# Optimization experiments

Measured on AMD Instinct MI355X. Metric: run time of the kernel, lower is better.

Reference implementation:

```python
import jax, jax.numpy as jnp
import numpy as np

B, T, C = 4, 2048, 1024
H = 16  # NUM_HEADS
HD = C // H  # head_dim = 64


def setup_inputs() -> dict:
    key = jax.random.key(0)
    k1, k2, k3 = jax.random.split(key, 3)
    x = jax.random.normal(k1, (B, T, C), dtype=jnp.float32)
    # nn.Linear weights: stored as [out, in]; apply as x @ W.T
    W_attn = jax.random.normal(k2, (3 * C, C), dtype=jnp.float32) * (1.0 / np.sqrt(C))
    W_proj = jax.random.normal(k3, (C, C), dtype=jnp.float32) * (1.0 / np.sqrt(C))
    return {"x": x, "W_attn": W_attn, "W_proj": W_proj}


def reference(x, W_attn, W_proj):
    Bv, Tv, Cv = x.shape
    qkv = x @ W_attn.T  # [B, T, 3C]
    q, k, v = jnp.split(qkv, 3, axis=2)
    # [B, H, T, HD]
    q = q.reshape(Bv, Tv, H, HD).transpose(0, 2, 1, 3)
    k = k.reshape(Bv, Tv, H, HD).transpose(0, 2, 1, 3)
    v = v.reshape(Bv, Tv, H, HD).transpose(0, 2, 1, 3)
    att = jnp.einsum("bhqd,bhkd->bhqk", q, k) * (1.0 / np.sqrt(HD))
    causal = jnp.tril(jnp.ones((Tv, Tv), dtype=bool))
    att = jnp.where(causal[None, None, :, :], att, -jnp.inf)
    att = jax.nn.softmax(att, axis=-1)
    y = jnp.einsum("bhqk,bhkd->bhqd", att, v)
    y = y.transpose(0, 2, 1, 3).reshape(Bv, Tv, Cv)
    return y @ W_proj.T
```

## Files before the change

### kernel.cpp

```cpp
#include <hip/hip_runtime.h>

typedef _Float16 f16;
typedef _Float16 half8 __attribute__((ext_vector_type(8)));
typedef _Float16 half4v __attribute__((ext_vector_type(4)));
typedef __fp16 fp16x2 __attribute__((ext_vector_type(2)));
typedef float floatx4 __attribute__((ext_vector_type(4)));
typedef unsigned int uint;

constexpr int Bsz = 4, Tseq = 2048, Cdim = 1024, NH = 16, HDim = 64;
constexpr int Mtok = Bsz * Tseq;
constexpr int NQT = Tseq / 64;
constexpr float QSCALE = 0.18033688f;

#define GLDS16(src, dst) __builtin_amdgcn_global_load_lds( \
    (const __attribute__((address_space(1))) void*)(src),  \
    (__attribute__((address_space(3))) void*)(dst), 16, 0, 0)

__device__ __forceinline__ float fexp2(float x) { return __builtin_amdgcn_exp2f(x); }
__device__ __forceinline__ uint pkrtz(float a, float b) {
  fp16x2 h = __builtin_amdgcn_cvt_pkrtz(a, b);
  return __builtin_bit_cast(uint, h);
}
#define MFMA16(a, b, c) __builtin_amdgcn_mfma_f32_16x16x32_f16((a), (b), (c), 0, 0, 0)

__global__ void cvt3_kernel(const float* __restrict__ x, const float* __restrict__ wa,
                            const float* __restrict__ wp,
                            f16* __restrict__ xh, f16* __restrict__ wah, f16* __restrict__ wph) {
  constexpr int nx = Mtok * Cdim, nwa = 3 * Cdim * Cdim, nwp = Cdim * Cdim;
  int i = (blockIdx.x * blockDim.x + threadIdx.x) * 4;
  const float* src; f16* dst; int off;
  if (i < nx)            { src = x;  dst = xh;  off = i; }
  else if (i < nx + nwa) { src = wa; dst = wah; off = i - nx; }
  else                   { src = wp; dst = wph; off = i - nx - nwa; }
  float4 v = *(const float4*)(src + off);
  half4v o;
  o[0] = (f16)v.x; o[1] = (f16)v.y; o[2] = (f16)v.z; o[3] = (f16)v.w;
  *(half4v*)(dst + off) = o;
}

__global__ __launch_bounds__(512, 2)
void qk8p_kernel(const f16* __restrict__ X, const f16* __restrict__ W,
                 f16* __restrict__ q_out, f16* __restrict__ k_out)
{
  __shared__ __align__(16) char smem[131072];
  constexpr int K = 1024, NT = 16;
  const int sbid = (blockIdx.x & 7) * 32 + (blockIdx.x >> 3);
  const int bm = sbid >> 3, bn = sbid & 7;
  const int m0 = bm * 256, n0 = bn * 256;
  const int tid = threadIdx.x, w = tid >> 6, lane = tid & 63;
  const int wr = w >> 2, wc = w & 3;
  const int g = lane >> 4, lm = lane & 15;

  const int grow = lane >> 3;
  const int cg = (lane & 7) ^ grow;

  auto stage_half = [&](int op, int t, int h) {
    const f16* src = op ? W : X;
    char* base = smem + op * 65536 + (t & 1) * 32768 + h * 16384;
    const int rbase = (op ? n0 : m0) + h * 128;
#pragma unroll
    for (int r2 = 0; r2 < 2; ++r2) {
      int row = rbase + r2 * 64 + w * 8 + grow;
      GLDS16(src + (size_t)row * K + t * 64 + cg * 8,
             base + (r2 * 64 + w * 8) * 128);
    }
  };

  floatx4 acc[8][4];
#pragma unroll
  for (int i = 0; i < 8; ++i)
#pragma unroll
    for (int j = 0; j < 4; ++j) acc[i][j] = (floatx4)0.0f;

  const int sw = lm & 7;
  const char* S = smem;
  const int Abase = wr * 16384 + lm * 128;
  const int Bbase = 65536 + (wc >> 1) * 16384 + ((wc & 1) * 64 + lm) * 128;

  half8 a0[4][2], a1[4][2], b0[2][2], b1[2][2];

  stage_half(0, 0, 0); stage_half(0, 0, 1);
  stage_half(1, 0, 0); stage_half(1, 0, 1);
  stage_half(1, 1, 0); stage_half(1, 1, 1);

#pragma unroll 2
  for (int t = 0; t < NT; ++t) {
    const int par = (t & 1) * 32768;

    if (t == NT - 1) { asm volatile("s_waitcnt vmcnt(0)" ::: "memory"); }
    else             { asm volatile("s_waitcnt vmcnt(4)" ::: "memory"); }
    __builtin_amdgcn_s_barrier();
#pragma unroll
    for (int i = 0; i < 4; ++i)
#pragma unroll
      for (int kk = 0; kk < 2; ++kk)
        a0[i][kk] = *(const half8*)(S + par + Abase + i * 2048 + 16 * ((kk * 4 + g) ^ sw));
#pragma unroll
    for (int j = 0; j < 2; ++j)
#pragma unroll
      for (int kk = 0; kk < 2; ++kk)
        b0[j][kk] = *(const half8*)(S + par + Bbase + j * 2048 + 16 * ((kk * 4 + g) ^ sw));
    if (t + 1 < NT) stage_half(0, t + 1, 0);
    asm volatile("s_waitcnt lgkmcnt(0)" ::: "memory");
    __builtin_amdgcn_sched_barrier(0);
    __builtin_amdgcn_s_setprio(1);
#pragma unroll
    for (int i = 0; i < 4; ++i)
#pragma unroll
      for (int j = 0; j < 2; ++j)
#pragma unroll
        for (int kk = 0; kk < 2; ++kk)
          acc[i][j] = MFMA16(a0[i][kk], b0[j][kk], acc[i][j]);
    __builtin_amdgcn_s_setprio(0);

    __builtin_amdgcn_s_barrier();
#pragma unroll
    for (int j = 0; j < 2; ++j)
#pragma unroll
      for (int kk = 0; kk < 2; ++kk)
        b1[j][kk] = *(const half8*)(S + par + Bbase + (j + 2) * 2048 + 16 * ((kk * 4 + g) ^ sw));
    if (t + 1 < NT) stage_half(0, t + 1, 1);
    asm volatile("s_waitcnt lgkmcnt(0)" ::: "memory");
    __builtin_amdgcn_sched_barrier(0);
    __builtin_amdgcn_s_setprio(1);
#pragma unroll
    for (int i = 0; i < 4; ++i)
#pragma unroll
      for (int j = 0; j < 2; ++j)
#pragma unroll
        for (int kk = 0; kk < 2; ++kk)
          acc[i][j + 2] = MFMA16(a0[i][kk], b1[j][kk], acc[i][j + 2]);
    __builtin_amdgcn_s_setprio(0);

    __builtin_amdgcn_s_barrier();
#pragma unroll
    for (int i = 0; i < 4; ++i)
#pragma unroll
      for (int kk = 0; kk < 2; ++kk)
        a1[i][kk] = *(const half8*)(S + par + Abase + (i + 4) * 2048 + 16 * ((kk * 4 + g) ^ sw));
    if (t + 2 < NT) stage_half(1, t + 2, 0);
    asm volatile("s_waitcnt lgkmcnt(0)" ::: "memory");
    __builtin_amdgcn_sched_barrier(0);
    __builtin_amdgcn_s_setprio(1);
#pragma unroll
    for (int i = 0; i < 4; ++i)
#pragma unroll
      for (int j = 0; j < 2; ++j)
#pragma unroll
        for (int kk = 0; kk < 2; ++kk)
          acc[i + 4][j + 2] = MFMA16(a1[i][kk], b1[j][kk], acc[i + 4][j + 2]);
    __builtin_amdgcn_s_setprio(0);

    __builtin_amdgcn_s_barrier();
    if (t + 2 < NT) stage_half(1, t + 2, 1);
    __builtin_amdgcn_s_setprio(1);
#pragma unroll
    for (int i = 0; i < 4; ++i)
#pragma unroll
      for (int j = 0; j < 2; ++j)
#pragma unroll
        for (int kk = 0; kk < 2; ++kk)
          acc[i + 4][j] = MFMA16(a1[i][kk], b0[j][kk], acc[i + 4][j]);
    __builtin_amdgcn_s_setprio(0);
  }

#pragma unroll
  for (int i = 0; i < 8; ++i) {
#pragma unroll
    for (int j = 0; j < 4; ++j) {
#pragma unroll
      for (int r = 0; r < 4; ++r) {
        int m = m0 + wr * 128 + i * 16 + 4 * g + r;
        int n = n0 + wc * 64 + j * 16 + lm;
        float v = acc[i][j][r];
        int which = n >> 10;
        int inner = n & 1023;
        int h = inner >> 6, hd = inner & 63;
        int b = m >> 11, t = m & 2047;
        if (which == 0) {
          v *= QSCALE;
          q_out[(((size_t)(b * NH + h)) * Tseq + t) * HDim + hd] = (f16)v;
        } else {
          k_out[(((size_t)(b * NH + h)) * Tseq + t) * HDim + hd] = (f16)v;
        }
      }
    }
  }
}

template<int EPI>
__device__ __forceinline__ void gemm_body(f16* As, f16* Bs,
    const f16* __restrict__ X, const f16* __restrict__ W,
    float* __restrict__ outF, f16* __restrict__ v_out,
    int N, int K, int bm, int bn)
{
  constexpr int BK = 32;
  const int tid = threadIdx.x;
  const int wave = tid >> 6;
  const int lane = tid & 63;
  const int g = lane >> 4, lm = lane & 15;
  const int m0 = bm * 128, n0 = bn * 128;
  const int wr = wave >> 1, wc = wave & 1;

  floatx4 acc[4][4];
#pragma unroll
  for (int i = 0; i < 4; ++i)
#pragma unroll
    for (int j = 0; j < 4; ++j) acc[i][j] = (floatx4)0.0f;

  for (int k0 = 0; k0 < K; k0 += BK) {
    __syncthreads();
#pragma unroll
    for (int t = 0; t < 2; ++t) {
      int row = (wave * 2 + t) * 16 + (lane >> 2);
      int cg = (lane & 3) ^ ((row >> 1) & 3);
      GLDS16(X + (size_t)(m0 + row) * K + k0 + cg * 8,
             (char*)As + (wave * 2 + t) * 1024);
      GLDS16(W + (size_t)(n0 + row) * K + k0 + cg * 8,
             (char*)Bs + (wave * 2 + t) * 1024);
    }
    __syncthreads();

    half8 af[4], bf[4];
#pragma unroll
    for (int i = 0; i < 4; ++i) {
      int rowa = wr * 64 + i * 16 + lm;
      int cga = g ^ ((rowa >> 1) & 3);
      af[i] = *(const half8*)((const char*)As + rowa * 64 + cga * 16);
      int rowb = wc * 64 + i * 16 + lm;
      int cgb = g ^ ((rowb >> 1) & 3);
      bf[i] = *(const half8*)((const char*)Bs + rowb * 64 + cgb * 16);
    }
#pragma unroll
    for (int i = 0; i < 4; ++i)
#pragma unroll
      for (int j = 0; j < 4; ++j)
        acc[i][j] = MFMA16(af[i], bf[j], acc[i][j]);
  }

#pragma unroll
  for (int i = 0; i < 4; ++i) {
#pragma unroll
    for (int j = 0; j < 4; ++j) {
#pragma unroll
      for (int r = 0; r < 4; ++r) {
        int m = m0 + wr * 64 + i * 16 + 4 * g + r;
        int n = n0 + wc * 64 + j * 16 + lm;
        float v = acc[i][j][r];
        if constexpr (EPI == 1) {
          outF[(size_t)m * N + n] = v;
        } else {
          int h = m >> 6, hd = m & 63;
          int b = n >> 11, t = n & 2047;
          v_out[(((size_t)(b * NH + h)) * HDim + hd) * Tseq + t] = (f16)v;
        }
      }
    }
  }
}

__global__ __launch_bounds__(256)
void vt_kernel(const f16* __restrict__ xh, const f16* __restrict__ wVh, f16* __restrict__ Vth) {
  __shared__ __align__(16) f16 As[128 * 32];
  __shared__ __align__(16) f16 Bs[128 * 32];
  int bm = blockIdx.x & 7, bn = blockIdx.x >> 3;
  gemm_body<2>(As, Bs, wVh, xh, nullptr, Vth, Mtok, Cdim, bm, bn);
}

__global__ __launch_bounds__(256)
void proj_kernel(const f16* __restrict__ yh, const f16* __restrict__ wPh, float* __restrict__ out) {
  __shared__ __align__(16) f16 As[128 * 32];
  __shared__ __align__(16) f16 Bs[128 * 32];
  const int x = blockIdx.x & 7;
  const int u = blockIdx.x >> 3;
  int c = u >> 4, ww = u & 15;
  int bm = x * 8 + (c >> 1) * 4 + (ww >> 2);
  int bn = (c & 1) * 4 + (ww & 3);
  gemm_body<1>(As, Bs, yh, wPh, out, nullptr, Cdim, Cdim, bm, bn);
}

__device__ __forceinline__ void softmax_tile(floatx4* s,
                                             bool diag, int j0, int qg, char* pwrow, int g, int lm) {
  if (diag) {
#pragma unroll
    for (int nf = 0; nf < 4; ++nf)
#pragma unroll
      for (int r = 0; r < 4; ++r)
        if (j0 + nf * 16 + 4 * g + r > qg) s[nf][r] = -1e30f;
  }
#pragma unroll
  for (int nf = 0; nf < 4; ++nf) {
    float p0 = fexp2(s[nf][0]), p1 = fexp2(s[nf][1]);
    float p2 = fexp2(s[nf][2]), p3 = fexp2(s[nf][3]);
    uint lo = pkrtz(p0, p1), hi = pkrtz(p2, p3);
    int slot = 2 * nf + (g >> 1);
    uint2 u; u.x = lo; u.y = hi;
    *(uint2*)(pwrow + 16 * (slot ^ (lm & 7)) + 8 * (g & 1)) = u;
  }
}

__device__ __forceinline__ void store_o(const floatx4* acc, const floatx4 l5, int q0w,
                                        int g, int lm, f16* __restrict__ Y, int b, int h) {
#pragma unroll
  for (int r = 0; r < 4; ++r) {
    float inv = 1.0f / l5[r];
    int t = q0w + 4 * g + r;
    size_t base = ((size_t)(b * Tseq + t)) * Cdim + h * HDim;
#pragma unroll
    for (int ng = 0; ng < 4; ++ng)
      Y[base + ng * 16 + lm] = (f16)(acc[ng][r] * inv);
  }
}

__global__ __launch_bounds__(256)
void attn_kernel(const f16* __restrict__ Q, const f16* __restrict__ Kg,
                 const f16* __restrict__ Vt, f16* __restrict__ Y)
{
  __shared__ __align__(16) char smem[40960];
  int wg = blockIdx.x;
  int lin = (wg & 7) * 128 + (wg >> 3);
  const int p  = lin & 15;
  const int bh = lin >> 4;
  const int itB = NQT - p;
  const f16* Qb  = Q  + (size_t)bh * Tseq * HDim;
  const f16* Kb  = Kg + (size_t)bh * Tseq * HDim;
  const f16* Vtb = Vt + (size_t)bh * HDim * Tseq;

  const int tid = threadIdx.x, w = tid >> 6, lane = tid & 63;
  const int g = lane >> 4, lm = lane & 15;
  char* pwrow = smem + 32768 + w * 2048 + lm * 128;
  const int b = bh >> 4, h = bh & 15;

  half8 ones;
#pragma unroll
  for (int i = 0; i < 8; ++i) ones[i] = (f16)1.0f;

  int q0 = (NQT - 1 - p) * 64;
  int qg = q0 + w * 16 + lm;
  half8 qf0 = *(const half8*)(Qb + (size_t)(q0 + w * 16 + lm) * HDim + g * 8);
  half8 qf1 = *(const half8*)(Qb + (size_t)(q0 + w * 16 + lm) * HDim + 32 + g * 8);

  floatx4 acc[4], acc5;
  acc5 = (floatx4)0.f;
#pragma unroll
  for (int ng = 0; ng < 4; ++ng) acc[ng] = (floatx4)0.f;

  const int srow = w * 8 + (lane >> 3);
  const int sslot = lane & 7;

  auto stage = [&](int j0s, int buf) {
#pragma unroll
    for (int t = 0; t < 2; ++t) {
      int row = srow + t * 32;
      int cg = sslot ^ (row & 7);
      GLDS16(Kb + (size_t)(j0s + row) * HDim + cg * 8,
             smem + buf * 8192 + (w * 8 + t * 32) * 128);
      GLDS16(Vtb + (size_t)row * Tseq + j0s + cg * 8,
             smem + 16384 + buf * 8192 + (w * 8 + t * 32) * 128);
    }
  };

  stage(0, 0);
  asm volatile("s_waitcnt vmcnt(0)" ::: "memory");
  __builtin_amdgcn_s_barrier();

  for (int it = 0; it < NQT + 1; ++it) {
    const bool lastB = (it == itB - 1);
    const bool last  = (it == NQT);
    const int jt = (it < itB) ? it : it - itB;
    const int j0 = jt * 64;

    if (!last) {
      const int itn = it + 1;
      const int jtn = (itn < itB) ? itn : itn - itB;
      stage(jtn * 64, itn & 1);
    }

    char* kb   = smem + (it & 1) * 8192;
    char* vbuf = smem + 16384 + (it & 1) * 8192;

    floatx4 s[4];
    __builtin_amdgcn_s_setprio(1);
#pragma unroll
    for (int nf = 0; nf < 4; ++nf) {
      half8 kf0 = *(const half8*)(kb + (nf * 16 + lm) * 128 + 16 * ((g)     ^ (lm & 7)));
      half8 kf1 = *(const half8*)(kb + (nf * 16 + lm) * 128 + 16 * ((4 + g) ^ (lm & 7)));
      s[nf] = MFMA16(kf0, qf0, (floatx4)0.f);
      s[nf] = MFMA16(kf1, qf1, s[nf]);
    }
    __builtin_amdgcn_s_setprio(0);

    softmax_tile(s, lastB || last, j0, qg, pwrow, g, lm);
    half8 pa0 = *(const half8*)(pwrow + 16 * ((g)     ^ (lm & 7)));
    half8 pa1 = *(const half8*)(pwrow + 16 * ((4 + g) ^ (lm & 7)));

    __builtin_amdgcn_s_setprio(1);
    acc5 = MFMA16(pa0, ones, acc5);
    acc5 = MFMA16(pa1, ones, acc5);
#pragma unroll
    for (int c = 0; c < 2; ++c)
#pragma unroll
      for (int ng = 0; ng < 4; ++ng) {
        half8 vbf = *(const half8*)(vbuf + (ng * 16 + lm) * 128 + 16 * ((4 * c + g) ^ (lm & 7)));
        acc[ng] = MFMA16(c ? pa1 : pa0, vbf, acc[ng]);
      }
    __builtin_amdgcn_s_setprio(0);

    asm volatile("s_waitcnt vmcnt(0)" ::: "memory");
    __builtin_amdgcn_s_barrier();

    if (lastB) {
      store_o(acc, acc5, q0 + 16 * w, g, lm, Y, b, h);
      q0 = p * 64;
      qg = q0 + w * 16 + lm;
      qf0 = *(const half8*)(Qb + (size_t)(q0 + w * 16 + lm) * HDim + g * 8);
      qf1 = *(const half8*)(Qb + (size_t)(q0 + w * 16 + lm) * HDim + 32 + g * 8);
      acc5 = (floatx4)0.f;
#pragma unroll
      for (int ng = 0; ng < 4; ++ng) acc[ng] = (floatx4)0.f;
    }
  }

  store_o(acc, acc5, q0 + 16 * w, g, lm, Y, b, h);
}

extern "C" void kernel_launch(void* const* d_in, const int* in_sizes, int n_in,
                              void* d_out, int out_size, void* d_ws, size_t ws_size,
                              hipStream_t stream)
{
  const float* x      = (const float*)d_in[0];
  const float* W_attn = (const float*)d_in[1];
  const float* W_proj = (const float*)d_in[2];
  float* out = (float*)d_out;

  char* ws = (char*)d_ws;
  f16* xh  = (f16*)(ws);
  f16* wAh = (f16*)(ws + (size_t)(16u << 20));
  f16* wPh = (f16*)(ws + (size_t)(22u << 20));
  f16* Qh  = (f16*)(ws + (size_t)(24u << 20));
  f16* Kh  = (f16*)(ws + (size_t)(40u << 20));
  f16* Vth = (f16*)(ws + (size_t)(56u << 20));
  f16* yh  = xh;

  constexpr int ntot = (Mtok * Cdim + 3 * Cdim * Cdim + Cdim * Cdim) / 4;
  cvt3_kernel<<<(ntot + 255) / 256, 256, 0, stream>>>(x, W_attn, W_proj, xh, wAh, wPh);

  qk8p_kernel<<<dim3(256), 512, 0, stream>>>(xh, wAh, Qh, Kh);

  vt_kernel<<<dim3(512), 256, 0, stream>>>(xh, wAh + (size_t)2048 * Cdim, Vth);

  attn_kernel<<<dim3(1024), 256, 0, stream>>>(Qh, Kh, Vth, yh);

  proj_kernel<<<dim3(512), 256, 0, stream>>>(yh, wPh, out);
}
```

Baseline: 168.2 us.

## Replace V and projection GEMMs with 8-wave double-buffered pipelined GEMM

Replaces the simple 4-wave 128x128 BK=32 GEMM used for the V-transpose and output projection with an 8-wave 128x256 tile using BK=64. The new kernel double-buffers LDS, prefetches the next k-tile with global_load_lds, and interleaves LDS reads with MFMA in four phases. It also uses explicit waitcnt, s_setprio and sched barriers. The aim is to hide global load latency, cut barrier stalls and raise MFMA utilization. In exchange it uses 96KB of LDS per block and needs careful manual vmcnt accounting.

Result: faster. 155.2 us (-7.7%).

```diff
diff --git a/kernel.cpp b/kernel.cpp
--- a/kernel.cpp
+++ b/kernel.cpp
@@ -189,18 +189,32 @@
 }
 
 template<int EPI>
-__device__ __forceinline__ void gemm_body(f16* As, f16* Bs,
-    const f16* __restrict__ X, const f16* __restrict__ W,
+__device__ __forceinline__ void g8p_body(char* smem,
+    const f16* __restrict__ A, const f16* __restrict__ B,
     float* __restrict__ outF, f16* __restrict__ v_out,
-    int N, int K, int bm, int bn)
+    int bm, int bn)
 {
-  constexpr int BK = 32;
-  const int tid = threadIdx.x;
-  const int wave = tid >> 6;
-  const int lane = tid & 63;
+  constexpr int K = 1024, NT = 16;
+  const int m0 = bm * 128, n0 = bn * 256;
+  const int tid = threadIdx.x, w = tid >> 6, lane = tid & 63;
+  const int wr = w >> 2, wc = w & 3;
   const int g = lane >> 4, lm = lane & 15;
-  const int m0 = bm * 128, n0 = bn * 128;
-  const int wr = wave >> 1, wc = wave & 1;
+  const int grow = lane >> 3;
+  const int cg = (lane & 7) ^ grow;
+
+  auto stage_A = [&](int t, int h) {
+    int row = m0 + h * 64 + w * 8 + grow;
+    GLDS16(A + (size_t)row * K + t * 64 + cg * 8,
+           smem + (t & 1) * 16384 + (h * 64 + w * 8) * 128);
+  };
+  auto stage_B = [&](int t, int h) {
+#pragma unroll
+    for (int r2 = 0; r2 < 2; ++r2) {
+      int row = n0 + h * 128 + r2 * 64 + w * 8 + grow;
+      GLDS16(B + (size_t)row * K + t * 64 + cg * 8,
+             smem + 32768 + (t & 1) * 32768 + (h * 128 + r2 * 64 + w * 8) * 128);
+    }
+  };
 
   floatx4 acc[4][4];
 #pragma unroll
@@ -208,34 +222,97 @@
 #pragma unroll
     for (int j = 0; j < 4; ++j) acc[i][j] = (floatx4)0.0f;
 
-  for (int k0 = 0; k0 < K; k0 += BK) {
-    __syncthreads();
-#pragma unroll
-    for (int t = 0; t < 2; ++t) {
-      int row = (wave * 2 + t) * 16 + (lane >> 2);
-      int cg = (lane & 3) ^ ((row >> 1) & 3);
-      GLDS16(X + (size_t)(m0 + row) * K + k0 + cg * 8,
-             (char*)As + (wave * 2 + t) * 1024);
-      GLDS16(W + (size_t)(n0 + row) * K + k0 + cg * 8,
-             (char*)Bs + (wave * 2 + t) * 1024);
-    }
-    __syncthreads();
-
-    half8 af[4], bf[4];
-#pragma unroll
-    for (int i = 0; i < 4; ++i) {
-      int rowa = wr * 64 + i * 16 + lm;
-      int cga = g ^ ((rowa >> 1) & 3);
-      af[i] = *(const half8*)((const char*)As + rowa * 64 + cga * 16);
-      int rowb = wc * 64 + i * 16 + lm;
-      int cgb = g ^ ((rowb >> 1) & 3);
-      bf[i] = *(const half8*)((const char*)Bs + rowb * 64 + cgb * 16);
-    }
-#pragma unroll
-    for (int i = 0; i < 4; ++i)
-#pragma unroll
-      for (int j = 0; j < 4; ++j)
-        acc[i][j] = MFMA16(af[i], bf[j], acc[i][j]);
+  const int sw = lm & 7;
+  const char* S = smem;
+  const int Abase = (wr * 64 + lm) * 128;
+  const int Bbase = 32768 + (wc * 64 + lm) * 128;
+
+  half8 a0[2][2], a1[2][2], b0[2][2], b1[2][2];
+
+  stage_A(0, 0); stage_A(0, 1);
+  stage_B(0, 0); stage_B(0, 1);
+  stage_B(1, 0); stage_B(1, 1);
+
+#pragma unroll 2
+  for (int t = 0; t < NT; ++t) {
+    const int parA = (t & 1) * 16384;
+    const int parB = (t & 1) * 32768;
+
+    if (t == NT - 1) { asm volatile("s_waitcnt vmcnt(0)" ::: "memory"); }
+    else             { asm volatile("s_waitcnt vmcnt(4)" ::: "memory"); }
+    __builtin_amdgcn_s_barrier();
+#pragma unroll
+    for (int i = 0; i < 2; ++i)
+#pragma unroll
+      for (int kk = 0; kk < 2; ++kk)
+        a0[i][kk] = *(const half8*)(S + parA + Abase + i * 2048 + 16 * ((kk * 4 + g) ^ sw));
+#pragma unroll
+    for (int j = 0; j < 2; ++j)
+#pragma unroll
+      for (int kk = 0; kk < 2; ++kk)
+        b0[j][kk] = *(const half8*)(S + parB + Bbase + j * 2048 + 16 * ((kk * 4 + g) ^ sw));
+    if (t + 1 < NT) stage_A(t + 1, 0);
+    asm volatile("s_waitcnt lgkmcnt(0)" ::: "memory");
+    __builtin_amdgcn_sched_barrier(0);
+    __builtin_amdgcn_s_setprio(1);
+#pragma unroll
+    for (int i = 0; i < 2; ++i)
+#pragma unroll
+      for (int j = 0; j < 2; ++j)
+#pragma unroll
+        for (int kk = 0; kk < 2; ++kk)
+          acc[i][j] = MFMA16(a0[i][kk], b0[j][kk], acc[i][j]);
+    __builtin_amdgcn_s_setprio(0);
+
+    __builtin_amdgcn_s_barrier();
+#pragma unroll
+    for (int j = 0; j < 2; ++j)
+#pragma unroll
+      for (int kk = 0; kk < 2; ++kk)
+        b1[j][kk] = *(const half8*)(S + parB + Bbase + (j + 2) * 2048 + 16 * ((kk * 4 + g) ^ sw));
+    if (t + 1 < NT) stage_A(t + 1, 1);
+    asm volatile("s_waitcnt lgkmcnt(0)" ::: "memory");
+    __builtin_amdgcn_sched_barrier(0);
+    __builtin_amdgcn_s_setprio(1);
+#pragma unroll
+    for (int i = 0; i < 2; ++i)
+#pragma unroll
+      for (int j = 0; j < 2; ++j)
+#pragma unroll
+        for (int kk = 0; kk < 2; ++kk)
+          acc[i][j + 2] = MFMA16(a0[i][kk], b1[j][kk], acc[i][j + 2]);
+    __builtin_amdgcn_s_setprio(0);
+
+    __builtin_amdgcn_s_barrier();
+#pragma unroll
+    for (int i = 0; i < 2; ++i)
+#pragma unroll
+      for (int kk = 0; kk < 2; ++kk)
+        a1[i][kk] = *(const half8*)(S + parA + Abase + (i + 2) * 2048 + 16 * ((kk * 4 + g) ^ sw));
+    if (t + 2 < NT) stage_B(t + 2, 0);
+    asm volatile("s_waitcnt lgkmcnt(0)" ::: "memory");
+    __builtin_amdgcn_sched_barrier(0);
+    __builtin_amdgcn_s_setprio(1);
+#pragma unroll
+    for (int i = 0; i < 2; ++i)
+#pragma unroll
+      for (int j = 0; j < 2; ++j)
+#pragma unroll
+        for (int kk = 0; kk < 2; ++kk)
+          acc[i + 2][j + 2] = MFMA16(a1[i][kk], b1[j][kk], acc[i + 2][j + 2]);
+    __builtin_amdgcn_s_setprio(0);
+
+    __builtin_amdgcn_s_barrier();
+    if (t + 2 < NT) stage_B(t + 2, 1);
+    __builtin_amdgcn_s_setprio(1);
+#pragma unroll
+    for (int i = 0; i < 2; ++i)
+#pragma unroll
+      for (int j = 0; j < 2; ++j)
+#pragma unroll
+        for (int kk = 0; kk < 2; ++kk)
+          acc[i + 2][j] = MFMA16(a1[i][kk], b0[j][kk], acc[i + 2][j]);
+    __builtin_amdgcn_s_setprio(0);
   }
 
 #pragma unroll
@@ -248,35 +325,33 @@
         int n = n0 + wc * 64 + j * 16 + lm;
         float v = acc[i][j][r];
         if constexpr (EPI == 1) {
-          outF[(size_t)m * N + n] = v;
+          outF[(size_t)m * Cdim + n] = v;
         } else {
           int h = m >> 6, hd = m & 63;
-          int b = n >> 11, t = n & 2047;
-          v_out[(((size_t)(b * NH + h)) * HDim + hd) * Tseq + t] = (f16)v;
+          int b = n >> 11, tt = n & 2047;
+          v_out[(((size_t)(b * NH + h)) * HDim + hd) * Tseq + tt] = (f16)v;
         }
       }
     }
   }
 }
 
-__global__ __launch_bounds__(256)
-void vt_kernel(const f16* __restrict__ xh, const f16* __restrict__ wVh, f16* __restrict__ Vth) {
-  __shared__ __align__(16) f16 As[128 * 32];
-  __shared__ __align__(16) f16 Bs[128 * 32];
-  int bm = blockIdx.x & 7, bn = blockIdx.x >> 3;
-  gemm_body<2>(As, Bs, wVh, xh, nullptr, Vth, Mtok, Cdim, bm, bn);
-}
-
-__global__ __launch_bounds__(256)
-void proj_kernel(const f16* __restrict__ yh, const f16* __restrict__ wPh, float* __restrict__ out) {
-  __shared__ __align__(16) f16 As[128 * 32];
-  __shared__ __align__(16) f16 Bs[128 * 32];
-  const int x = blockIdx.x & 7;
-  const int u = blockIdx.x >> 3;
-  int c = u >> 4, ww = u & 15;
-  int bm = x * 8 + (c >> 1) * 4 + (ww >> 2);
-  int bn = (c & 1) * 4 + (ww & 3);
-  gemm_body<1>(As, Bs, yh, wPh, out, nullptr, Cdim, Cdim, bm, bn);
+__global__ __launch_bounds__(512, 2)
+void vt8p_kernel(const f16* __restrict__ xh, const f16* __restrict__ wVh, f16* __restrict__ Vth) {
+  __shared__ __align__(16) char smem[98304];
+  const int x = blockIdx.x & 7, q = blockIdx.x >> 3;
+  int bn = x * 4 + (q >> 3);
+  int bm = q & 7;
+  g8p_body<2>(smem, wVh, xh, nullptr, Vth, bm, bn);
+}
+
+__global__ __launch_bounds__(512, 2)
+void proj8p_kernel(const f16* __restrict__ yh, const f16* __restrict__ wPh, float* __restrict__ out) {
+  __shared__ __align__(16) char smem[98304];
+  const int x = blockIdx.x & 7, q = blockIdx.x >> 3;
+  int bm = x * 8 + (q >> 2);
+  int bn = q & 3;
+  g8p_body<1>(smem, yh, wPh, out, nullptr, bm, bn);
 }
 
 __device__ __forceinline__ void softmax_tile(floatx4* s,
@@ -447,9 +522,9 @@
 
   qk8p_kernel<<<dim3(256), 512, 0, stream>>>(xh, wAh, Qh, Kh);
 
-  vt_kernel<<<dim3(512), 256, 0, stream>>>(xh, wAh + (size_t)2048 * Cdim, Vth);
+  vt8p_kernel<<<dim3(256), 512, 0, stream>>>(xh, wAh + (size_t)2048 * Cdim, Vth);
 
   attn_kernel<<<dim3(1024), 256, 0, stream>>>(Qh, Kh, Vth, yh);
 
-  proj_kernel<<<dim3(512), 256, 0, stream>>>(yh, wPh, out);
-}
+  proj8p_kernel<<<dim3(256), 512, 0, stream>>>(yh, wPh, out);
+}
```
